# Performance work log

Measured on AMD Instinct MI355X. Metric: run time of the kernel, lower is better.

The kernel has to match this reference:

```python
import jax, jax.numpy as jnp
import numpy as np

N = 50000      # nodes
E = 800000     # edges (avg degree 16)
IN_DIM = 128
H = 8          # num_heads
D = 16         # out_dim per head


def setup_inputs() -> dict:
    key = jax.random.key(0)
    ks = jax.random.split(key, 10)
    s = 1.0 / np.sqrt(IN_DIM)
    return {
        "h_src": jax.random.normal(ks[0], (N, IN_DIM), jnp.float32),
        "h_dst": jax.random.normal(ks[1], (N, IN_DIM), jnp.float32),
        "src": jax.random.randint(ks[2], (E,), 0, N),
        "dst": jax.random.randint(ks[3], (E,), 0, N),
        "Qw": jax.random.normal(ks[4], (IN_DIM, H * D), jnp.float32) * s,
        "Qb": jnp.zeros((H * D,), jnp.float32),
        "Kw": jax.random.normal(ks[5], (IN_DIM, H * D), jnp.float32) * s,
        "Kb": jnp.zeros((H * D,), jnp.float32),
        "Vw": jax.random.normal(ks[6], (IN_DIM, H * D), jnp.float32) * s,
        "Vb": jnp.zeros((H * D,), jnp.float32),
    }


def reference(h_src, h_dst, src, dst, Qw, Qb, Kw, Kb, Vw, Vb):
    # Node-level projections: [N, H, D]
    Q = (h_dst @ Qw + Qb).reshape(-1, H, D)
    K = (h_src @ Kw + Kb).reshape(-1, H, D)
    V = (h_src @ Vw + Vb).reshape(-1, H, D)
    # Edge-wise dot product per head: [E, H, 1]
    score = jnp.sum(K[src] * Q[dst], axis=-1, keepdims=True)
    # exp of clamped scaled score (note: clamp(-5,5) BEFORE exp, as in scaled_exp)
    score = jnp.exp(jnp.clip(score / jnp.float32(np.sqrt(D)), -5.0, 5.0))
    # Scatter-sum aggregation onto destination nodes
    wV = jax.ops.segment_sum(score * V[src], dst, num_segments=N)  # [N, H, D]
    z = jax.ops.segment_sum(score, dst, num_segments=N)            # [N, H, 1]
    return wV / z
```

## Files before the change

kernel.cpp:

```cpp
#include <hip/hip_runtime.h>
#include <hip/hip_bf16.h>
#include <math.h>

#define N_NODES 50000
#define E_EDGES 800000
#define IN_DIM  128
#define HD      128
#define SQRT_D_INV 0.25f

#define PROJ_BLOCKS ((N_NODES + 63) / 64)
#define HIST_BLOCKS 1024

typedef __attribute__((ext_vector_type(8))) short short8v;
typedef __attribute__((ext_vector_type(4))) float float4v;

__device__ inline unsigned short f2bf(float x) {
    __hip_bfloat16 b = __float2bfloat16(x);
    return *reinterpret_cast<unsigned short*>(&b);
}
__device__ inline float bflo(unsigned int u) { return __uint_as_float(u << 16); }
__device__ inline float bfhi(unsigned int u) { return __uint_as_float(u & 0xffff0000u); }

__global__ __launch_bounds__(256) void wtr_kernel(
    const float* __restrict__ Qw, const float* __restrict__ Kw, const float* __restrict__ Vw,
    unsigned short* __restrict__ wt)
{
    int i = blockIdx.x * 256 + threadIdx.x;
    int which = i >> 14;
    int r = i & 16383;
    int k = r >> 7, n = r & 127;
    const float* W = (which == 0) ? Qw : (which == 1) ? Kw : Vw;
    wt[((size_t)which << 14) + n * 128 + k] = f2bf(W[r]);
}

__global__ __launch_bounds__(256) void proj_hist_kernel(
    const float* __restrict__ h_src, const float* __restrict__ h_dst,
    const unsigned short* __restrict__ wt,
    const float* __restrict__ Qb, const float* __restrict__ Kb, const float* __restrict__ Vb,
    unsigned short* __restrict__ qkv,
    const int* __restrict__ dst, int* __restrict__ counts, int* __restrict__ rank)
{
    if (blockIdx.x >= PROJ_BLOCKS) {
        int tid = (blockIdx.x - PROJ_BLOCKS) * 256 + threadIdx.x;
        for (int e = tid; e < E_EDGES; e += HIST_BLOCKS * 256)
            rank[e] = atomicAdd(&counts[dst[e]], 1);
        return;
    }

    __shared__ __align__(16) short sbuf[4][4224];
    const int t  = threadIdx.x;
    const int wv = t >> 6;
    const int l  = t & 63;
    const int lr = l & 15;
    const int kg = l >> 4;
    const int m_base = blockIdx.x * 64 + wv * 16;
    const int arow = min(m_base + lr, N_NODES - 1);

    const float* pd = h_dst + (size_t)arow * IN_DIM;
    const float* ps = h_src + (size_t)arow * IN_DIM;

    short8v afd[4], afs[4];
    #pragma unroll
    for (int ks = 0; ks < 4; ++ks) {
        const int k0 = ks * 32 + kg * 8;
        float4 a0 = *(const float4*)&pd[k0];
        float4 a1 = *(const float4*)&pd[k0 + 4];
        float4 b0 = *(const float4*)&ps[k0];
        float4 b1 = *(const float4*)&ps[k0 + 4];
        afd[ks][0] = (short)f2bf(a0.x); afd[ks][1] = (short)f2bf(a0.y);
        afd[ks][2] = (short)f2bf(a0.z); afd[ks][3] = (short)f2bf(a0.w);
        afd[ks][4] = (short)f2bf(a1.x); afd[ks][5] = (short)f2bf(a1.y);
        afd[ks][6] = (short)f2bf(a1.z); afd[ks][7] = (short)f2bf(a1.w);
        afs[ks][0] = (short)f2bf(b0.x); afs[ks][1] = (short)f2bf(b0.y);
        afs[ks][2] = (short)f2bf(b0.z); afs[ks][3] = (short)f2bf(b0.w);
        afs[ks][4] = (short)f2bf(b1.x); afs[ks][5] = (short)f2bf(b1.y);
        afs[ks][6] = (short)f2bf(b1.z); afs[ks][7] = (short)f2bf(b1.w);
    }

    unsigned short* buf = (unsigned short*)&sbuf[wv][0];

    {
        float4v acc[8];
        #pragma unroll
        for (int i = 0; i < 8; ++i) acc[i] = (float4v)0.f;
        #pragma unroll
        for (int ks = 0; ks < 4; ++ks) {
            const int k0 = ks * 32 + kg * 8;
            #pragma unroll
            for (int nf = 0; nf < 8; ++nf) {
                short8v bf = *(const short8v*)&wt[(size_t)(nf * 16 + lr) * 128 + k0];
                acc[nf] = __builtin_amdgcn_mfma_f32_16x16x32_bf16(afd[ks], bf, acc[nf], 0, 0, 0);
            }
        }
        #pragma unroll
        for (int nf = 0; nf < 8; ++nf) {
            const float b = Qb[nf * 16 + lr];
            #pragma unroll
            for (int r = 0; r < 4; ++r)
                buf[(kg * 4 + r) * 136 + nf * 16 + lr] = f2bf(acc[nf][r] + b);
        }
    }
    __syncthreads();
    #pragma unroll
    for (int i = 0; i < 4; ++i) {
        const int chunk = i * 64 + l;
        const int row = chunk >> 4;
        const int c   = (chunk & 15) * 8;
        const int m = m_base + row;
        short8v v = *(const short8v*)&buf[row * 136 + c];
        if (m < N_NODES) *(short8v*)&qkv[(size_t)m * 384 + c] = v;
    }
    __syncthreads();

    {
        float4v accK[8], accV[8];
        #pragma unroll
        for (int i = 0; i < 8; ++i) { accK[i] = (float4v)0.f; accV[i] = (float4v)0.f; }
        const unsigned short* WK = wt + (1 << 14);
        const unsigned short* WV = wt + (2 << 14);
        #pragma unroll
        for (int ks = 0; ks < 4; ++ks) {
            const int k0 = ks * 32 + kg * 8;
            #pragma unroll
            for (int nf = 0; nf < 8; ++nf) {
                short8v bk = *(const short8v*)&WK[(size_t)(nf * 16 + lr) * 128 + k0];
                short8v bv = *(const short8v*)&WV[(size_t)(nf * 16 + lr) * 128 + k0];
                accK[nf] = __builtin_amdgcn_mfma_f32_16x16x32_bf16(afs[ks], bk, accK[nf], 0, 0, 0);
                accV[nf] = __builtin_amdgcn_mfma_f32_16x16x32_bf16(afs[ks], bv, accV[nf], 0, 0, 0);
            }
        }
        #pragma unroll
        for (int nf = 0; nf < 8; ++nf) {
            const float bk = Kb[nf * 16 + lr], bv = Vb[nf * 16 + lr];
            #pragma unroll
            for (int r = 0; r < 4; ++r) {
                buf[(kg * 4 + r) * 264 + nf * 16 + lr]       = f2bf(accK[nf][r] + bk);
                buf[(kg * 4 + r) * 264 + 128 + nf * 16 + lr] = f2bf(accV[nf][r] + bv);
            }
        }
    }
    __syncthreads();
    #pragma unroll
    for (int i = 0; i < 8; ++i) {
        const int chunk = i * 64 + l;
        const int row = chunk >> 5;
        const int c   = (chunk & 31) * 8;
        const int m = m_base + row;
        short8v v = *(const short8v*)&buf[row * 264 + c];
        if (m < N_NODES) *(short8v*)&qkv[(size_t)m * 384 + 128 + c] = v;
    }
}

__global__ __launch_bounds__(256) void offsets_kernel(const int* __restrict__ counts,
                                                      int* __restrict__ beg,
                                                      int* __restrict__ total) {
    int i = blockIdx.x * blockDim.x + threadIdx.x;
    int lane = threadIdx.x & 63;
    int v = (i < N_NODES) ? counts[i] : 0;
    int incl = v;
    #pragma unroll
    for (int off = 1; off < 64; off <<= 1) {
        int y = __shfl_up(incl, off);
        if (lane >= off) incl += y;
    }
    int wsum = __shfl(incl, 63);
    int base = 0;
    if (lane == 0) base = atomicAdd(total, wsum);
    base = __shfl(base, 0);
    if (i < N_NODES) beg[i] = base + incl - v;
}

__global__ void scatter_kernel(const int* __restrict__ src, const int* __restrict__ dst,
                               const int* __restrict__ beg, const int* __restrict__ rank,
                               int* __restrict__ esrc) {
    int e = blockIdx.x * blockDim.x + threadIdx.x;
    if (e < E_EDGES) esrc[beg[dst[e]] + rank[e]] = src[e];
}

__global__ __launch_bounds__(256) void agg_kernel(
    const unsigned short* __restrict__ qkv,
    const int* __restrict__ begp, const int* __restrict__ cntp,
    const int* __restrict__ esrc, float* __restrict__ out)
{
    int wave = (blockIdx.x * blockDim.x + threadIdx.x) >> 6;
    const int lane = threadIdx.x & 63;
    if (wave >= N_NODES) return;
    const int n = __builtin_amdgcn_readfirstlane(wave);
    const int e = lane >> 4;
    const int u = lane & 15;

    const uint4 qv = *(const uint4*)&qkv[(size_t)n * 384 + u * 8];
    const float q0 = bflo(qv.x), q1 = bfhi(qv.x), q2 = bflo(qv.y), q3 = bfhi(qv.y);
    const float q4 = bflo(qv.z), q5 = bfhi(qv.z), q6 = bflo(qv.w), q7 = bfhi(qv.w);

    const int b0 = begp[n], c0 = cntp[n], endp = b0 + c0;

    float a0=0.f,a1=0.f,a2=0.f,a3=0.f,a4=0.f,a5=0.f,a6=0.f,a7=0.f, z=0.f;

    for (int base = b0; base < endp; base += 4) {
        const int i  = base + e;
        const int iv = min(i, endp - 1);
        const int s  = esrc[iv];
        const size_t ro = (size_t)s * 384;
        const uint4 kk = *(const uint4*)&qkv[ro + 128 + u * 8];
        const uint4 vv = *(const uint4*)&qkv[ro + 256 + u * 8];
        float d =      q0 * bflo(kk.x);
        d = fmaf(q1, bfhi(kk.x), d);
        d = fmaf(q2, bflo(kk.y), d);
        d = fmaf(q3, bfhi(kk.y), d);
        d = fmaf(q4, bflo(kk.z), d);
        d = fmaf(q5, bfhi(kk.z), d);
        d = fmaf(q6, bflo(kk.w), d);
        d = fmaf(q7, bfhi(kk.w), d);
        d += __shfl_xor(d, 1);
        float sc = __expf(fminf(fmaxf(d * SQRT_D_INV, -5.f), 5.f));
        float w = (i < endp) ? sc : 0.f;
        z += w;
        a0 = fmaf(w, bflo(vv.x), a0);
        a1 = fmaf(w, bfhi(vv.x), a1);
        a2 = fmaf(w, bflo(vv.y), a2);
        a3 = fmaf(w, bfhi(vv.y), a3);
        a4 = fmaf(w, bflo(vv.z), a4);
        a5 = fmaf(w, bfhi(vv.z), a5);
        a6 = fmaf(w, bflo(vv.w), a6);
        a7 = fmaf(w, bfhi(vv.w), a7);
    }

    #pragma unroll
    for (int mask = 16; mask <= 32; mask <<= 1) {
        z  += __shfl_xor(z, mask);
        a0 += __shfl_xor(a0, mask);
        a1 += __shfl_xor(a1, mask);
        a2 += __shfl_xor(a2, mask);
        a3 += __shfl_xor(a3, mask);
        a4 += __shfl_xor(a4, mask);
        a5 += __shfl_xor(a5, mask);
        a6 += __shfl_xor(a6, mask);
        a7 += __shfl_xor(a7, mask);
    }

    const float inv = 1.f / z;
    if (e == 0) {
        *(float4*)&out[(size_t)n * HD + u * 8]     = make_float4(a0*inv, a1*inv, a2*inv, a3*inv);
        *(float4*)&out[(size_t)n * HD + u * 8 + 4] = make_float4(a4*inv, a5*inv, a6*inv, a7*inv);
    }
}

extern "C" void kernel_launch(void* const* d_in, const int* in_sizes, int n_in,
                              void* d_out, int out_size, void* d_ws, size_t ws_size,
                              hipStream_t stream) {
    const float* h_src = (const float*)d_in[0];
    const float* h_dst = (const float*)d_in[1];
    const int*   src   = (const int*)d_in[2];
    const int*   dst   = (const int*)d_in[3];
    const float* Qw    = (const float*)d_in[4];
    const float* Qb    = (const float*)d_in[5];
    const float* Kw    = (const float*)d_in[6];
    const float* Kb    = (const float*)d_in[7];
    const float* Vw    = (const float*)d_in[8];
    const float* Vb    = (const float*)d_in[9];
    float* out = (float*)d_out;

    char* ws = (char*)d_ws;
    const size_t qkv_bytes = (size_t)N_NODES * 384 * sizeof(unsigned short);
    const size_t wt_bytes  = 3 * 128 * 128 * sizeof(unsigned short);
    unsigned short* qkvp = (unsigned short*)(ws);
    unsigned short* wtp  = (unsigned short*)(ws + qkv_bytes);
    int* counts = (int*)(ws + qkv_bytes + wt_bytes);
    int* total  = counts + N_NODES;
    int* beg    = total + 1;
    int* rank   = beg + N_NODES;
    int* esrc   = rank + E_EDGES;

    hipMemsetAsync(counts, 0, (N_NODES + 1) * sizeof(int), stream);

    wtr_kernel<<<192, 256, 0, stream>>>(Qw, Kw, Vw, wtp);

    proj_hist_kernel<<<PROJ_BLOCKS + HIST_BLOCKS, 256, 0, stream>>>(
        h_src, h_dst, wtp, Qb, Kb, Vb, qkvp, dst, counts, rank);

    offsets_kernel<<<(N_NODES + 255) / 256, 256, 0, stream>>>(counts, beg, total);

    scatter_kernel<<<(E_EDGES + 255) / 256, 256, 0, stream>>>(src, dst, beg, rank, esrc);

    agg_kernel<<<(N_NODES * 64 + 255) / 256, 256, 0, stream>>>(qkvp, beg, counts, esrc, out);
}
```

Measured before the change: 165.1 us.

## Stage projection weights in swizzled LDS, fuse memset, unroll aggregation loop

The projection kernel now loads each 128x128 bf16 weight matrix into XOR-swizzled shared memory once per block and runs Q, K and V as three sequential phases, instead of every wave reading B fragments from global memory. The histogram blocks move to the front of the grid so the atomic counting is scheduled first. The counts memset is folded into the weight-transpose kernel, removing one API call. The aggregation loop handles two edge batches per iteration to raise memory-level parallelism. In exchange, the larger LDS footprint (32KB) may reduce occupancy, and the extra barriers serialise the phases.

```diff
diff --git a/kernel.cpp b/kernel.cpp
--- a/kernel.cpp
+++ b/kernel.cpp
@@ -21,16 +21,19 @@
 __device__ inline float bflo(unsigned int u) { return __uint_as_float(u << 16); }
 __device__ inline float bfhi(unsigned int u) { return __uint_as_float(u & 0xffff0000u); }
 
-__global__ __launch_bounds__(256) void wtr_kernel(
+__global__ __launch_bounds__(256) void wtr_init_kernel(
     const float* __restrict__ Qw, const float* __restrict__ Kw, const float* __restrict__ Vw,
-    unsigned short* __restrict__ wt)
+    unsigned short* __restrict__ wt, int* __restrict__ counts)
 {
     int i = blockIdx.x * 256 + threadIdx.x;
-    int which = i >> 14;
-    int r = i & 16383;
-    int k = r >> 7, n = r & 127;
-    const float* W = (which == 0) ? Qw : (which == 1) ? Kw : Vw;
-    wt[((size_t)which << 14) + n * 128 + k] = f2bf(W[r]);
+    if (i <= N_NODES) counts[i] = 0;
+    if (i < 3 * 16384) {
+        int which = i >> 14;
+        int r = i & 16383;
+        int k = r >> 7, n = r & 127;
+        const float* W = (which == 0) ? Qw : (which == 1) ? Kw : Vw;
+        wt[((size_t)which << 14) + n * 128 + k] = f2bf(W[r]);
+    }
 }
 
 __global__ __launch_bounds__(256) void proj_hist_kernel(
@@ -40,20 +43,20 @@
     unsigned short* __restrict__ qkv,
     const int* __restrict__ dst, int* __restrict__ counts, int* __restrict__ rank)
 {
-    if (blockIdx.x >= PROJ_BLOCKS) {
-        int tid = (blockIdx.x - PROJ_BLOCKS) * 256 + threadIdx.x;
+    if (blockIdx.x < HIST_BLOCKS) {
+        int tid = blockIdx.x * 256 + threadIdx.x;
         for (int e = tid; e < E_EDGES; e += HIST_BLOCKS * 256)
             rank[e] = atomicAdd(&counts[dst[e]], 1);
         return;
     }
 
-    __shared__ __align__(16) short sbuf[4][4224];
+    __shared__ __align__(16) unsigned short smem[16384];
     const int t  = threadIdx.x;
     const int wv = t >> 6;
     const int l  = t & 63;
     const int lr = l & 15;
     const int kg = l >> 4;
-    const int m_base = blockIdx.x * 64 + wv * 16;
+    const int m_base = (blockIdx.x - HIST_BLOCKS) * 64 + wv * 16;
     const int arow = min(m_base + lr, N_NODES - 1);
 
     const float* pd = h_dst + (size_t)arow * IN_DIM;
@@ -77,77 +80,54 @@
         afs[ks][6] = (short)f2bf(b1.z); afs[ks][7] = (short)f2bf(b1.w);
     }
 
-    unsigned short* buf = (unsigned short*)&sbuf[wv][0];
-
-    {
+    unsigned short* stg = &smem[wv * 4224];
+
+    #pragma unroll
+    for (int phase = 0; phase < 3; ++phase) {
+        if (phase) __syncthreads();
+        const unsigned short* wsrc = wt + ((size_t)phase << 14);
+        #pragma unroll
+        for (int j = 0; j < 8; ++j) {
+            const int selem = j * 2048 + t * 8;
+            const int d = selem * 2;
+            const int sd = d ^ (((d >> 8) & 7) << 4);
+            *(short8v*)((char*)smem + sd) = *(const short8v*)&wsrc[selem];
+        }
+        __syncthreads();
+
+        const short8v* aF = (phase == 0) ? afd : afs;
         float4v acc[8];
         #pragma unroll
         for (int i = 0; i < 8; ++i) acc[i] = (float4v)0.f;
         #pragma unroll
         for (int ks = 0; ks < 4; ++ks) {
-            const int k0 = ks * 32 + kg * 8;
             #pragma unroll
             for (int nf = 0; nf < 8; ++nf) {
-                short8v bf = *(const short8v*)&wt[(size_t)(nf * 16 + lr) * 128 + k0];
-                acc[nf] = __builtin_amdgcn_mfma_f32_16x16x32_bf16(afd[ks], bf, acc[nf], 0, 0, 0);
+                const int a = (nf * 16 + lr) * 256 + ks * 64 + kg * 16;
+                const int sa = a ^ ((lr & 7) << 4);
+                short8v bf = *(const short8v*)((const char*)smem + sa);
+                acc[nf] = __builtin_amdgcn_mfma_f32_16x16x32_bf16(aF[ks], bf, acc[nf], 0, 0, 0);
             }
         }
+        __syncthreads();
+
+        const float* bias = (phase == 0) ? Qb : (phase == 1) ? Kb : Vb;
         #pragma unroll
         for (int nf = 0; nf < 8; ++nf) {
-            const float b = Qb[nf * 16 + lr];
+            const float b = bias[nf * 16 + lr];
             #pragma unroll
             for (int r = 0; r < 4; ++r)
-                buf[(kg * 4 + r) * 136 + nf * 16 + lr] = f2bf(acc[nf][r] + b);
-        }
-    }
-    __syncthreads();
-    #pragma unroll
-    for (int i = 0; i < 4; ++i) {
-        const int chunk = i * 64 + l;
-        const int row = chunk >> 4;
-        const int c   = (chunk & 15) * 8;
-        const int m = m_base + row;
-        short8v v = *(const short8v*)&buf[row * 136 + c];
-        if (m < N_NODES) *(short8v*)&qkv[(size_t)m * 384 + c] = v;
-    }
-    __syncthreads();
-
-    {
-        float4v accK[8], accV[8];
-        #pragma unroll
-        for (int i = 0; i < 8; ++i) { accK[i] = (float4v)0.f; accV[i] = (float4v)0.f; }
-        const unsigned short* WK = wt + (1 << 14);
-        const unsigned short* WV = wt + (2 << 14);
-        #pragma unroll
-        for (int ks = 0; ks < 4; ++ks) {
-            const int k0 = ks * 32 + kg * 8;
-            #pragma unroll
-            for (int nf = 0; nf < 8; ++nf) {
-                short8v bk = *(const short8v*)&WK[(size_t)(nf * 16 + lr) * 128 + k0];
-                short8v bv = *(const short8v*)&WV[(size_t)(nf * 16 + lr) * 128 + k0];
-                accK[nf] = __builtin_amdgcn_mfma_f32_16x16x32_bf16(afs[ks], bk, accK[nf], 0, 0, 0);
-                accV[nf] = __builtin_amdgcn_mfma_f32_16x16x32_bf16(afs[ks], bv, accV[nf], 0, 0, 0);
-            }
-        }
-        #pragma unroll
-        for (int nf = 0; nf < 8; ++nf) {
-            const float bk = Kb[nf * 16 + lr], bv = Vb[nf * 16 + lr];
-            #pragma unroll
-            for (int r = 0; r < 4; ++r) {
-                buf[(kg * 4 + r) * 264 + nf * 16 + lr]       = f2bf(accK[nf][r] + bk);
-                buf[(kg * 4 + r) * 264 + 128 + nf * 16 + lr] = f2bf(accV[nf][r] + bv);
-            }
-        }
-    }
-    __syncthreads();
-    #pragma unroll
-    for (int i = 0; i < 8; ++i) {
-        const int chunk = i * 64 + l;
-        const int row = chunk >> 5;
-        const int c   = (chunk & 31) * 8;
-        const int m = m_base + row;
-        short8v v = *(const short8v*)&buf[row * 264 + c];
-        if (m < N_NODES) *(short8v*)&qkv[(size_t)m * 384 + 128 + c] = v;
+                stg[(kg * 4 + r) * 136 + nf * 16 + lr] = f2bf(acc[nf][r] + b);
+        }
+        #pragma unroll
+        for (int i = 0; i < 4; ++i) {
+            const int chunk = i * 64 + l;
+            const int row = chunk >> 4;
+            const int c   = (chunk & 15) * 8;
+            const int m = m_base + row;
+            short8v v = *(const short8v*)&stg[row * 136 + c];
+            if (m < N_NODES) *(short8v*)&qkv[(size_t)m * 384 + phase * 128 + c] = v;
+        }
     }
 }
 
@@ -197,33 +177,56 @@
 
     float a0=0.f,a1=0.f,a2=0.f,a3=0.f,a4=0.f,a5=0.f,a6=0.f,a7=0.f, z=0.f;
 
-    for (int base = b0; base < endp; base += 4) {
-        const int i  = base + e;
-        const int iv = min(i, endp - 1);
-        const int s  = esrc[iv];
-        const size_t ro = (size_t)s * 384;
-        const uint4 kk = *(const uint4*)&qkv[ro + 128 + u * 8];
-        const uint4 vv = *(const uint4*)&qkv[ro + 256 + u * 8];
-        float d =      q0 * bflo(kk.x);
-        d = fmaf(q1, bfhi(kk.x), d);
-        d = fmaf(q2, bflo(kk.y), d);
-        d = fmaf(q3, bfhi(kk.y), d);
-        d = fmaf(q4, bflo(kk.z), d);
-        d = fmaf(q5, bfhi(kk.z), d);
-        d = fmaf(q6, bflo(kk.w), d);
-        d = fmaf(q7, bfhi(kk.w), d);
-        d += __shfl_xor(d, 1);
-        float sc = __expf(fminf(fmaxf(d * SQRT_D_INV, -5.f), 5.f));
-        float w = (i < endp) ? sc : 0.f;
-        z += w;
-        a0 = fmaf(w, bflo(vv.x), a0);
-        a1 = fmaf(w, bfhi(vv.x), a1);
-        a2 = fmaf(w, bflo(vv.y), a2);
-        a3 = fmaf(w, bfhi(vv.y), a3);
-        a4 = fmaf(w, bflo(vv.z), a4);
-        a5 = fmaf(w, bfhi(vv.z), a5);
-        a6 = fmaf(w, bflo(vv.w), a6);
-        a7 = fmaf(w, bfhi(vv.w), a7);
+    for (int base = b0; base < endp; base += 8) {
+        const int i0 = base + e;
+        const int i1 = base + 4 + e;
+        const int s0 = esrc[min(i0, endp - 1)];
+        const int s1 = esrc[min(i1, endp - 1)];
+        const size_t r0 = (size_t)s0 * 384, r1 = (size_t)s1 * 384;
+        const uint4 kk0 = *(const uint4*)&qkv[r0 + 128 + u * 8];
+        const uint4 vv0 = *(const uint4*)&qkv[r0 + 256 + u * 8];
+        const uint4 kk1 = *(const uint4*)&qkv[r1 + 128 + u * 8];
+        const uint4 vv1 = *(const uint4*)&qkv[r1 + 256 + u * 8];
+
+        float d0 =      q0 * bflo(kk0.x);
+        d0 = fmaf(q1, bfhi(kk0.x), d0);
+        d0 = fmaf(q2, bflo(kk0.y), d0);
+        d0 = fmaf(q3, bfhi(kk0.y), d0);
+        d0 = fmaf(q4, bflo(kk0.z), d0);
+        d0 = fmaf(q5, bfhi(kk0.z), d0);
+        d0 = fmaf(q6, bflo(kk0.w), d0);
+        d0 = fmaf(q7, bfhi(kk0.w), d0);
+        d0 += __shfl_xor(d0, 1);
+        float w0 = (i0 < endp) ? __expf(fminf(fmaxf(d0 * SQRT_D_INV, -5.f), 5.f)) : 0.f;
+        z += w0;
+        a0 = fmaf(w0, bflo(vv0.x), a0);
+        a1 = fmaf(w0, bfhi(vv0.x), a1);
+        a2 = fmaf(w0, bflo(vv0.y), a2);
+        a3 = fmaf(w0, bfhi(vv0.y), a3);
+        a4 = fmaf(w0, bflo(vv0.z), a4);
+        a5 = fmaf(w0, bfhi(vv0.z), a5);
+        a6 = fmaf(w0, bflo(vv0.w), a6);
+        a7 = fmaf(w0, bfhi(vv0.w), a7);
+
+        float d1 =      q0 * bflo(kk1.x);
+        d1 = fmaf(q1, bfhi(kk1.x), d1);
+        d1 = fmaf(q2, bflo(kk1.y), d1);
+        d1 = fmaf(q3, bfhi(kk1.y), d1);
+        d1 = fmaf(q4, bflo(kk1.z), d1);
+        d1 = fmaf(q5, bfhi(kk1.z), d1);
+        d1 = fmaf(q6, bflo(kk1.w), d1);
+        d1 = fmaf(q7, bfhi(kk1.w), d1);
+        d1 += __shfl_xor(d1, 1);
+        float w1 = (i1 < endp) ? __expf(fminf(fmaxf(d1 * SQRT_D_INV, -5.f), 5.f)) : 0.f;
+        z += w1;
+        a0 = fmaf(w1, bflo(vv1.x), a0);
+        a1 = fmaf(w1, bfhi(vv1.x), a1);
+        a2 = fmaf(w1, bflo(vv1.y), a2);
+        a3 = fmaf(w1, bfhi(vv1.y), a3);
+        a4 = fmaf(w1, bflo(vv1.z), a4);
+        a5 = fmaf(w1, bfhi(vv1.z), a5);
+        a6 = fmaf(w1, bflo(vv1.w), a6);
+        a7 = fmaf(w1, bfhi(vv1.w), a7);
     }
 
     #pragma unroll
@@ -272,11 +275,9 @@
     int* rank   = beg + N_NODES;
     int* esrc   = rank + E_EDGES;
 
-    hipMemsetAsync(counts, 0, (N_NODES + 1) * sizeof(int), stream);
-
-    wtr_kernel<<<192, 256, 0, stream>>>(Qw, Kw, Vw, wtp);
-
-    proj_hist_kernel<<<PROJ_BLOCKS + HIST_BLOCKS, 256, 0, stream>>>(
+    wtr_init_kernel<<<196, 256, 0, stream>>>(Qw, Kw, Vw, wtp, counts);
+
+    proj_hist_kernel<<<HIST_BLOCKS + PROJ_BLOCKS, 256, 0, stream>>>(
         h_src, h_dst, wtp, Qb, Kb, Vb, qkvp, dst, counts, rank);
 
     offsets_kernel<<<(N_NODES + 255) / 256, 256, 0, stream>>>(counts, beg, total);
```

After: 142.9 us. 1.15x faster.
